# Optimization experiments

Hardware: AMD Instinct MI355X
Metric: run time of the kernel (lower is better)

The kernel has to match this reference:

```python
import jax, jax.numpy as jnp
import numpy as np

B, N, E = 1, 100000, 1250000
IN, OUT = 128, 64


def setup_inputs() -> dict:
    key = jax.random.key(0)
    k = jax.random.split(key, 5)
    x = jax.random.normal(k[0], (B, N, IN), jnp.float32)
    edge_index = jax.random.randint(k[1], (B, 2, E), 0, N, dtype=jnp.int32)
    rank_mapping = jnp.zeros((2, E), jnp.int32)  # single-rank: all zeros
    W1 = jax.random.normal(k[2], (IN, OUT), jnp.float32) / np.sqrt(IN)
    Wp = jax.random.normal(k[3], (2 * OUT, 1), jnp.float32) / np.sqrt(2 * OUT)
    bp = jnp.zeros((1,), jnp.float32)
    bias = jnp.zeros((OUT,), jnp.float32)
    return {"x": x, "edge_index": edge_index, "rank_mapping": rank_mapping,
            "W1": W1, "Wp": Wp, "bp": bp, "bias": bias}


def reference(x, edge_index, rank_mapping, W1, Wp, bp, bias):
    # x: [B, N, IN]; edge_index: [B, 2, E]
    del rank_mapping  # comm routing metadata; identity on a single rank
    n = x.shape[1]
    h = jnp.einsum('bnf,fo->bno', x, W1)          # conv1 (no bias)
    src = edge_index[:, 0, :]                     # [B, E]
    dst = edge_index[:, 1, :]
    h_i = jnp.take_along_axis(h, dst[..., None], axis=1)   # gather at dst
    h_j = jnp.take_along_axis(h, src[..., None], axis=1)   # gather at src
    messages = jnp.concatenate([h_i, h_j], axis=-1)        # [B, E, 2*OUT]
    s = jnp.einsum('bec,co->beo', messages, Wp) + bp       # project_message
    s = jnp.where(s >= 0, s, 0.2 * s)                      # LeakyReLU(0.2)
    numerator = jnp.exp(s)                                 # [B, E, 1]
    seg = jax.vmap(lambda v, i: jax.ops.segment_sum(v, i, num_segments=n))
    denominator = seg(numerator, dst)                      # [B, N, 1]
    # NOTE: original gathers denominator with the *src* indices — replicated.
    denom_e = jnp.take_along_axis(denominator, src[..., None], axis=1)
    alpha = numerator / (denom_e + 1e-16)                  # [B, E, 1]
    out = seg(h_j * alpha, dst)                            # scatter-aggregate
    return out + bias
```

## Files before the change

kernel.cpp:

```cpp
#include <hip/hip_runtime.h>


#define MAXB 1024
#define EPB 4096
#define BIN_CAP 2560

typedef __attribute__((ext_vector_type(8))) short short8v;
typedef __attribute__((ext_vector_type(4))) float floatx4;

static __device__ __forceinline__ float bf2f(unsigned short u) {
    unsigned v = (unsigned)u << 16;
    return __builtin_bit_cast(float, v);
}
static __device__ __forceinline__ unsigned short f2bf(float f) {
    unsigned u = __builtin_bit_cast(unsigned, f);
    u = (u + 0x7FFFu + ((u >> 16) & 1u)) >> 16;
    return (unsigned short)u;
}

__global__ __launch_bounds__(256) void fused_nt_count_kernel(
    const float* __restrict__ x, const float* __restrict__ W1,
    const float* __restrict__ Wp, const int* __restrict__ ei,
    float* __restrict__ h, float* __restrict__ aArr, float* __restrict__ bArr,
    int* __restrict__ C, int N, int E, int G, int B)
{
    __shared__ __align__(16) unsigned short w1b[4][4][4][16][8];
    __shared__ int cnt[MAXB];
    const int tid = threadIdx.x;

    if (blockIdx.x < G) {
        const int g = blockIdx.x;
        for (int i = tid; i < B; i += 256) cnt[i] = 0;
        __syncthreads();
        const int base = g * EPB;
        #pragma unroll
        for (int k = 0; k < EPB / 256; ++k) {
            int e = base + k * 256 + tid;
            if (e < E) atomicAdd(&cnt[ei[E + e] >> 7], 1);
        }
        __syncthreads();
        for (int i = tid; i < B; i += 256) C[(size_t)g * B + i] = cnt[i];
        return;
    }

    for (int i = tid; i < 128 * 64; i += 256) {
        int k = i >> 6, o = i & 63;
        w1b[k >> 5][o >> 4][(k >> 3) & 3][o & 15][k & 7] = f2bf(W1[i]);
    }

    const int w = tid >> 6, lane = tid & 63;
    const int hi = lane >> 4, col = lane & 15;
    float wpa4[4], wpb4[4];
    #pragma unroll
    for (int ot = 0; ot < 4; ++ot) {
        wpa4[ot] = Wp[ot * 16 + col];
        wpb4[ot] = Wp[64 + ot * 16 + col];
    }
    __syncthreads();

    const int n0 = (blockIdx.x - G) * 64 + w * 16;
    int arow = n0 + col; if (arow >= N) arow = N - 1;
    const float* xrow = x + (size_t)arow * 128 + hi * 8;

    floatx4 acc[4] = {{0.f,0.f,0.f,0.f},{0.f,0.f,0.f,0.f},
                      {0.f,0.f,0.f,0.f},{0.f,0.f,0.f,0.f}};
    #pragma unroll
    for (int kb = 0; kb < 4; ++kb) {
        float4 x0 = *reinterpret_cast<const float4*>(xrow + kb * 32);
        float4 x1 = *reinterpret_cast<const float4*>(xrow + kb * 32 + 4);
        short8v af;
        af[0] = (short)f2bf(x0.x); af[1] = (short)f2bf(x0.y);
        af[2] = (short)f2bf(x0.z); af[3] = (short)f2bf(x0.w);
        af[4] = (short)f2bf(x1.x); af[5] = (short)f2bf(x1.y);
        af[6] = (short)f2bf(x1.z); af[7] = (short)f2bf(x1.w);
        #pragma unroll
        for (int ot = 0; ot < 4; ++ot) {
            short8v bf = *reinterpret_cast<const short8v*>(&w1b[kb][ot][hi][col][0]);
            acc[ot] = __builtin_amdgcn_mfma_f32_16x16x32_bf16(af, bf, acc[ot], 0, 0, 0);
        }
    }

    #pragma unroll
    for (int ot = 0; ot < 4; ++ot) {
        #pragma unroll
        for (int r = 0; r < 4; ++r) {
            int n = n0 + hi * 4 + r;
            if (n < N) h[(size_t)n * 64 + ot * 16 + col] = acc[ot][r];
        }
    }
    #pragma unroll
    for (int r = 0; r < 4; ++r) {
        float pa = acc[0][r] * wpa4[0] + acc[1][r] * wpa4[1]
                 + acc[2][r] * wpa4[2] + acc[3][r] * wpa4[3];
        float pb = acc[0][r] * wpb4[0] + acc[1][r] * wpb4[1]
                 + acc[2][r] * wpb4[2] + acc[3][r] * wpb4[3];
        #pragma unroll
        for (int m = 1; m <= 8; m <<= 1) {
            pa += __shfl_xor(pa, m);
            pb += __shfl_xor(pb, m);
        }
        int n = n0 + hi * 4 + r;
        if (col == r && n < N) { aArr[n] = pa; bArr[n] = pb; }
    }
}

__global__ __launch_bounds__(256) void colscan_kernel(
    int* __restrict__ C, int* __restrict__ S, int G, int B)
{
    __shared__ int s[256];
    const int b = blockIdx.x, t = threadIdx.x;
    int g0 = 2 * t, g1 = 2 * t + 1;
    int c0 = (g0 < G) ? C[(size_t)g0 * B + b] : 0;
    int c1 = (g1 < G) ? C[(size_t)g1 * B + b] : 0;
    int v = c0 + c1;
    s[t] = v;
    __syncthreads();
    for (int off = 1; off < 256; off <<= 1) {
        int u = (t >= off) ? s[t - off] : 0;
        __syncthreads();
        s[t] += u;
        __syncthreads();
    }
    int ex = s[t] - v;
    if (g0 < G) C[(size_t)g0 * B + b] = ex;
    if (g1 < G) C[(size_t)g1 * B + b] = ex + c0;
    if (t == 255) S[b] = s[255];
}

__global__ __launch_bounds__(256) void binscan_kernel(
    const int* __restrict__ S, int* __restrict__ binStart,
    int* __restrict__ offsets, int B, int N, int E)
{
    __shared__ int ts[256];
    const int t = threadIdx.x;
    const int chunk = (B + 255) >> 8;
    const int base = t * chunk, lim = min(B, base + chunk);
    int s = 0;
    for (int i = base; i < lim; ++i) s += S[i];
    ts[t] = s;
    __syncthreads();
    for (int off = 1; off < 256; off <<= 1) {
        int u = (t >= off) ? ts[t - off] : 0;
        __syncthreads();
        ts[t] += u;
        __syncthreads();
    }
    int run = ts[t] - s;
    for (int i = base; i < lim; ++i) { binStart[i] = run; run += S[i]; }
    if (t == 0) { binStart[B] = E; offsets[N] = E; }
}

__global__ __launch_bounds__(1024) void pass2_kernel(
    const int* __restrict__ ei, const float* __restrict__ aArr,
    const float* __restrict__ bArr, const float* __restrict__ bp,
    const int* __restrict__ C, const int* __restrict__ binStart,
    int2* __restrict__ staging, int E, int G, int B)
{
    __shared__ int cur[MAXB];
    const int g = blockIdx.x, t = threadIdx.x;
    for (int i = t; i < B; i += 1024)
        cur[i] = binStart[i] + C[(size_t)g * B + i];
    __syncthreads();
    const float bp0 = bp[0];
    const int base = g * EPB;
    #pragma unroll
    for (int k = 0; k < EPB / 1024; ++k) {
        int e = base + k * 1024 + t;
        if (e >= E) break;
        int src = ei[e];
        int dst = ei[E + e];
        float s = aArr[dst] + bArr[src] + bp0;
        s = (s >= 0.f) ? s : 0.2f * s;
        float num = __expf(s);
        int bin = dst >> 7;
        int pos = atomicAdd(&cur[bin], 1);
        staging[pos] = make_int2(((dst & 127) << 17) | src, __float_as_int(num));
    }
}

__global__ __launch_bounds__(256) void localsort_kernel(
    const int* __restrict__ binStart, int2* __restrict__ staging,
    int* __restrict__ offsets, float* __restrict__ h, int N)
{
    __shared__ int2 sEnt[BIN_CAP];
    __shared__ int sCnt[256], sScan[256], sCur[128];
    __shared__ float dsum[128];
    const int b = blockIdx.x, t = threadIdx.x;
    const int sBeg = binStart[b];
    const int count = min(binStart[b + 1] - sBeg, BIN_CAP);

    sCnt[t] = 0;
    if (t < 128) { sCur[t] = 0; dsum[t] = 0.f; }
    __syncthreads();
    for (int i = t; i < count; i += 256) {
        int2 e = staging[sBeg + i];
        sEnt[i] = e;
        int dl = e.x >> 17;
        atomicAdd(&sCnt[dl], 1);
        atomicAdd(&dsum[dl], __int_as_float(e.y));
    }
    __syncthreads();
    int v = sCnt[t];
    sScan[t] = v;
    __syncthreads();
    for (int off = 1; off < 256; off <<= 1) {
        int u = (t >= off) ? sScan[t - off] : 0;
        __syncthreads();
        sScan[t] += u;
        __syncthreads();
    }
    int ex = sScan[t] - v;
    __syncthreads();
    sScan[t] = ex;
    const int n0 = b << 7;
    const int Cl = min(128, N - n0);
    if (t < Cl) offsets[n0 + t] = sBeg + ex;
    __syncthreads();
    for (int i = t; i < count; i += 256) {
        int2 e = sEnt[i];
        int dl = e.x >> 17;
        int pos = sBeg + sScan[dl] + atomicAdd(&sCur[dl], 1);
        staging[pos] = make_int2(e.x & 0x1FFFF, e.y);
    }

    const int wv_ = t >> 6, ln = t & 63;
    for (int dl = wv_; dl < Cl; dl += 4) {
        int n = n0 + dl;
        float inv = 1.f / (dsum[dl] + 1e-16f);
        float hv = h[(size_t)n * 64 + ln];
        asm volatile("" ::: "memory");
        reinterpret_cast<unsigned short*>(h)[(size_t)n * 128 + ln] = f2bf(hv * inv);
    }
}

__global__ __launch_bounds__(256) void aggregate_kernel(
    const int* __restrict__ offsets, const int2* __restrict__ sortedPair,
    const uint2* __restrict__ hhQ, const float* __restrict__ bias,
    float* __restrict__ out, int N)
{
    int gw = (blockIdx.x * blockDim.x + threadIdx.x) >> 6;
    int lane = threadIdx.x & 63;
    if (gw >= N) return;
    int beg = offsets[gw], end = offsets[gw + 1];
    const int quarter = lane >> 4;
    const int cg = lane & 15;
    float a0 = 0.f, a1 = 0.f, a2 = 0.f, a3 = 0.f;
    for (int e0 = beg; e0 < end; e0 += 64) {
        int idx = e0 + lane;
        int2 p = (idx < end) ? sortedPair[idx] : make_int2(0, 0);
        int cnt = min(64, end - e0);
        int j = 0;
        for (; j + 16 <= cnt; j += 16) {
            #pragma unroll
            for (int u = 0; u < 4; ++u) {
                int jj = j + 4 * u + quarter;
                int s = __shfl(p.x, jj);
                float wv = __shfl(__int_as_float(p.y), jj);
                uint2 g = hhQ[(size_t)s * 32 + cg];
                a0 = fmaf(bf2f((unsigned short)(g.x & 0xFFFFu)), wv, a0);
                a1 = fmaf(bf2f((unsigned short)(g.x >> 16)), wv, a1);
                a2 = fmaf(bf2f((unsigned short)(g.y & 0xFFFFu)), wv, a2);
                a3 = fmaf(bf2f((unsigned short)(g.y >> 16)), wv, a3);
            }
        }
        for (; j < cnt; j += 4) {
            int jj = j + quarter;
            int s = __shfl(p.x, jj);
            float wv = __shfl(__int_as_float(p.y), jj);
            uint2 g = hhQ[(size_t)s * 32 + cg];
            a0 = fmaf(bf2f((unsigned short)(g.x & 0xFFFFu)), wv, a0);
            a1 = fmaf(bf2f((unsigned short)(g.x >> 16)), wv, a1);
            a2 = fmaf(bf2f((unsigned short)(g.y & 0xFFFFu)), wv, a2);
            a3 = fmaf(bf2f((unsigned short)(g.y >> 16)), wv, a3);
        }
    }
    a0 += __shfl_xor(a0, 16); a0 += __shfl_xor(a0, 32);
    a1 += __shfl_xor(a1, 16); a1 += __shfl_xor(a1, 32);
    a2 += __shfl_xor(a2, 16); a2 += __shfl_xor(a2, 32);
    a3 += __shfl_xor(a3, 16); a3 += __shfl_xor(a3, 32);
    if (lane < 16) {
        float4 bq = reinterpret_cast<const float4*>(bias)[cg];
        float4 o;
        o.x = a0 + bq.x; o.y = a1 + bq.y; o.z = a2 + bq.z; o.w = a3 + bq.w;
        reinterpret_cast<float4*>(out)[(size_t)gw * 16 + cg] = o;
    }
}

extern "C" void kernel_launch(void* const* d_in, const int* in_sizes, int n_in,
                              void* d_out, int out_size, void* d_ws, size_t ws_size,
                              hipStream_t stream) {
    const float* x    = (const float*)d_in[0];
    const int*   ei   = (const int*)d_in[1];
    const float* W1   = (const float*)d_in[3];
    const float* Wp   = (const float*)d_in[4];
    const float* bp   = (const float*)d_in[5];
    const float* bias = (const float*)d_in[6];
    float* out = (float*)d_out;

    const int N = in_sizes[0] / 128;
    const int E = in_sizes[1] / 2;
    const int B = (N + 127) >> 7;
    const int G = (E + EPB - 1) / EPB;
    const int NTB = (N + 63) / 64;

    float* h        = (float*)d_ws;
    float* aArr     = h + (size_t)N * 64;
    float* bArr     = aArr + N;
    int*   C        = (int*)(bArr + N);
    int*   S        = C + (size_t)G * B;
    int*   binStart = S + B;
    int*   offsets  = binStart + (B + 1);
    int*   stRaw    = offsets + (N + 1);
    stRaw = (int*)(((uintptr_t)stRaw + 7) & ~(uintptr_t)7);
    int2*  staging  = (int2*)stRaw;

    fused_nt_count_kernel<<<G + NTB, 256, 0, stream>>>(
        x, W1, Wp, ei, h, aArr, bArr, C, N, E, G, B);

    colscan_kernel<<<B, 256, 0, stream>>>(C, S, G, B);

    binscan_kernel<<<1, 256, 0, stream>>>(S, binStart, offsets, B, N, E);

    pass2_kernel<<<G, 1024, 0, stream>>>(ei, aArr, bArr, bp, C, binStart,
                                         staging, E, G, B);

    localsort_kernel<<<B, 256, 0, stream>>>(binStart, staging, offsets, h, N);

    aggregate_kernel<<<(N * 64 + 255) / 256, 256, 0, stream>>>(
        offsets, staging, reinterpret_cast<const uint2*>(h), bias, out, N);
}
```

Measured before the change: 127.1 us.

## Pack normalized bf16 features densely and reorder edge-chunk prefix scan order

The normalized bf16 copy of h now goes to a separate dense buffer with a 128-byte row stride instead of being written in place into the fp32 rows with a 256-byte stride. This halves the footprint the random gathers in aggregation touch and improves cache-line use. The edge-chunk count grid is padded to a multiple of eight, and the column scan visits chunks in an interleaved order (8*(i%gp)+i/gp), which changes the order in which chunks fill each bin. That reorder looks aimed at how chunks are spread across the XCDs, at the cost of index arithmetic and extra workspace.

```diff
diff --git a/kernel.cpp b/kernel.cpp
--- a/kernel.cpp
+++ b/kernel.cpp
@@ -22,13 +22,13 @@
     const float* __restrict__ x, const float* __restrict__ W1,
     const float* __restrict__ Wp, const int* __restrict__ ei,
     float* __restrict__ h, float* __restrict__ aArr, float* __restrict__ bArr,
-    int* __restrict__ C, int N, int E, int G, int B)
+    int* __restrict__ C, int N, int E, int G8, int B)
 {
     __shared__ __align__(16) unsigned short w1b[4][4][4][16][8];
     __shared__ int cnt[MAXB];
     const int tid = threadIdx.x;
 
-    if (blockIdx.x < G) {
+    if (blockIdx.x < G8) {
         const int g = blockIdx.x;
         for (int i = tid; i < B; i += 256) cnt[i] = 0;
         __syncthreads();
@@ -58,7 +58,7 @@
     }
     __syncthreads();
 
-    const int n0 = (blockIdx.x - G) * 64 + w * 16;
+    const int n0 = (blockIdx.x - G8) * 64 + w * 16;
     int arow = n0 + col; if (arow >= N) arow = N - 1;
     const float* xrow = x + (size_t)arow * 128 + hi * 8;
 
@@ -105,13 +105,16 @@
 }
 
 __global__ __launch_bounds__(256) void colscan_kernel(
-    int* __restrict__ C, int* __restrict__ S, int G, int B)
+    int* __restrict__ C, int* __restrict__ S, int G8, int B)
 {
     __shared__ int s[256];
     const int b = blockIdx.x, t = threadIdx.x;
-    int g0 = 2 * t, g1 = 2 * t + 1;
-    int c0 = (g0 < G) ? C[(size_t)g0 * B + b] : 0;
-    int c1 = (g1 < G) ? C[(size_t)g1 * B + b] : 0;
+    const int gp = G8 >> 3;
+    int i0 = 2 * t, i1 = 2 * t + 1;
+    int ga = 8 * (i0 % gp) + (i0 / gp);
+    int gb = 8 * (i1 % gp) + (i1 / gp);
+    int c0 = (i0 < G8) ? C[(size_t)ga * B + b] : 0;
+    int c1 = (i1 < G8) ? C[(size_t)gb * B + b] : 0;
     int v = c0 + c1;
     s[t] = v;
     __syncthreads();
@@ -122,8 +125,8 @@
         __syncthreads();
     }
     int ex = s[t] - v;
-    if (g0 < G) C[(size_t)g0 * B + b] = ex;
-    if (g1 < G) C[(size_t)g1 * B + b] = ex + c0;
+    if (i0 < G8) C[(size_t)ga * B + b] = ex;
+    if (i1 < G8) C[(size_t)gb * B + b] = ex + c0;
     if (t == 255) S[b] = s[255];
 }
 
@@ -154,7 +157,7 @@
     const int* __restrict__ ei, const float* __restrict__ aArr,
     const float* __restrict__ bArr, const float* __restrict__ bp,
     const int* __restrict__ C, const int* __restrict__ binStart,
-    int2* __restrict__ staging, int E, int G, int B)
+    int2* __restrict__ staging, int E, int B)
 {
     __shared__ int cur[MAXB];
     const int g = blockIdx.x, t = threadIdx.x;
@@ -180,7 +183,8 @@
 
 __global__ __launch_bounds__(256) void localsort_kernel(
     const int* __restrict__ binStart, int2* __restrict__ staging,
-    int* __restrict__ offsets, float* __restrict__ h, int N)
+    int* __restrict__ offsets, const float* __restrict__ h,
+    unsigned short* __restrict__ hhD, int N)
 {
     __shared__ int2 sEnt[BIN_CAP];
     __shared__ int sCnt[256], sScan[256], sCur[128];
@@ -227,9 +231,7 @@
     for (int dl = wv_; dl < Cl; dl += 4) {
         int n = n0 + dl;
         float inv = 1.f / (dsum[dl] + 1e-16f);
-        float hv = h[(size_t)n * 64 + ln];
-        asm volatile("" ::: "memory");
-        reinterpret_cast<unsigned short*>(h)[(size_t)n * 128 + ln] = f2bf(hv * inv);
+        hhD[(size_t)n * 64 + ln] = f2bf(h[(size_t)n * 64 + ln] * inv);
     }
 }
 
@@ -256,7 +258,7 @@
                 int jj = j + 4 * u + quarter;
                 int s = __shfl(p.x, jj);
                 float wv = __shfl(__int_as_float(p.y), jj);
-                uint2 g = hhQ[(size_t)s * 32 + cg];
+                uint2 g = hhQ[(size_t)s * 16 + cg];
                 a0 = fmaf(bf2f((unsigned short)(g.x & 0xFFFFu)), wv, a0);
                 a1 = fmaf(bf2f((unsigned short)(g.x >> 16)), wv, a1);
                 a2 = fmaf(bf2f((unsigned short)(g.y & 0xFFFFu)), wv, a2);
@@ -267,7 +269,7 @@
             int jj = j + quarter;
             int s = __shfl(p.x, jj);
             float wv = __shfl(__int_as_float(p.y), jj);
-            uint2 g = hhQ[(size_t)s * 32 + cg];
+            uint2 g = hhQ[(size_t)s * 16 + cg];
             a0 = fmaf(bf2f((unsigned short)(g.x & 0xFFFFu)), wv, a0);
             a1 = fmaf(bf2f((unsigned short)(g.x >> 16)), wv, a1);
             a2 = fmaf(bf2f((unsigned short)(g.y & 0xFFFFu)), wv, a2);
@@ -301,31 +303,33 @@
     const int E = in_sizes[1] / 2;
     const int B = (N + 127) >> 7;
     const int G = (E + EPB - 1) / EPB;
+    const int G8 = (G + 7) & ~7;
     const int NTB = (N + 63) / 64;
 
     float* h        = (float*)d_ws;
     float* aArr     = h + (size_t)N * 64;
     float* bArr     = aArr + N;
     int*   C        = (int*)(bArr + N);
-    int*   S        = C + (size_t)G * B;
+    int*   S        = C + (size_t)G8 * B;
     int*   binStart = S + B;
     int*   offsets  = binStart + (B + 1);
     int*   stRaw    = offsets + (N + 1);
     stRaw = (int*)(((uintptr_t)stRaw + 7) & ~(uintptr_t)7);
     int2*  staging  = (int2*)stRaw;
-
-    fused_nt_count_kernel<<<G + NTB, 256, 0, stream>>>(
-        x, W1, Wp, ei, h, aArr, bArr, C, N, E, G, B);
-
-    colscan_kernel<<<B, 256, 0, stream>>>(C, S, G, B);
+    unsigned short* hhD = (unsigned short*)(staging + E);
+
+    fused_nt_count_kernel<<<G8 + NTB, 256, 0, stream>>>(
+        x, W1, Wp, ei, h, aArr, bArr, C, N, E, G8, B);
+
+    colscan_kernel<<<B, 256, 0, stream>>>(C, S, G8, B);
 
     binscan_kernel<<<1, 256, 0, stream>>>(S, binStart, offsets, B, N, E);
 
-    pass2_kernel<<<G, 1024, 0, stream>>>(ei, aArr, bArr, bp, C, binStart,
-                                         staging, E, G, B);
-
-    localsort_kernel<<<B, 256, 0, stream>>>(binStart, staging, offsets, h, N);
+    pass2_kernel<<<G8, 1024, 0, stream>>>(ei, aArr, bArr, bp, C, binStart,
+                                          staging, E, B);
+
+    localsort_kernel<<<B, 256, 0, stream>>>(binStart, staging, offsets, h, hhD, N);
 
     aggregate_kernel<<<(N * 64 + 255) / 256, 256, 0, stream>>>(
-        offsets, staging, reinterpret_cast<const uint2*>(h), bias, out, N);
-}
+        offsets, staging, reinterpret_cast<const uint2*>(hhD), bias, out, N);
+}
```

Measured after the change: 127.9 us. About the same (+0.6%).
